# Performance work log

Hardware: AMD Instinct MI355X
Metric: run time of the kernel (lower is better)

The kernel has to match this reference:

```python
import jax, jax.numpy as jnp
import numpy as np

N_NODES = 100000
N_EDGES = 1600000
D = 128  # node_feat_size == edge_hidden_size


def setup_inputs() -> dict:
    key = jax.random.key(0)
    ks = jax.random.split(key, 10)
    s = 1.0 / np.sqrt(D)
    return {
        "node_feats": jax.random.normal(ks[0], (N_NODES, D), jnp.float32),
        "edge_logits": jax.random.normal(ks[1], (N_EDGES, 1), jnp.float32),
        "W_proj": jax.random.normal(ks[2], (D, D), jnp.float32) * s,
        "b_proj": jax.random.normal(ks[3], (D,), jnp.float32) * s,
        "W1": jax.random.normal(ks[4], (2 * D, D), jnp.float32) * s,
        "b1": jax.random.normal(ks[5], (D,), jnp.float32) * s,
        "W2": jax.random.normal(ks[6], (D, D), jnp.float32) * s,
        "b2": jax.random.normal(ks[7], (D,), jnp.float32) * s,
        "src": jax.random.randint(ks[8], (N_EDGES,), 0, N_NODES),
        "dst": jax.random.randint(ks[9], (N_EDGES,), 0, N_NODES),
    }


def reference(node_feats, edge_logits, W_proj, b_proj, W1, b1, W2, b2, src, dst):
    # ---- edge_softmax: softmax of edge_logits grouped by destination node ----
    # [E,1] logits; per-dst max for numerical stability (gradient-free shift)
    m = jax.ops.segment_max(edge_logits, dst, num_segments=N_NODES)  # [N,1]
    m = jnp.where(jnp.isfinite(m), m, 0.0)  # nodes with no in-edges
    e = jnp.exp(edge_logits - jax.lax.stop_gradient(m)[dst])  # [E,1]
    z = jax.ops.segment_sum(e, dst, num_segments=N_NODES)  # [N,1]
    a = e / z[dst]  # [E,1]

    # ---- project_node (dropout is identity at inference) ----
    hv = node_feats @ W_proj + b_proj  # [N,D]

    # ---- src_mul_edge + sum aggregation: c[v] = sum_{(u->v)} a_uv * hv[u] ----
    msg = hv[src] * a  # [E,D]
    c = jax.ops.segment_sum(msg, dst, num_segments=N_NODES)  # [N,D]

    context = jax.nn.elu(c)
    x = jnp.concatenate([context, node_feats], axis=1)  # [N,2D]
    h = jax.nn.relu(x @ W1 + b1)  # Linear -> Dropout(id) -> ReLU
    out = jax.nn.relu(h @ W2 + b2)  # Linear -> Dropout(id), outer ReLU
    return out
```

## Files before the change

### kernel.cpp

```cpp
#include <hip/hip_runtime.h>
#include <hip/hip_bf16.h>

typedef __hip_bfloat16 bf16;
typedef __attribute__((ext_vector_type(8))) __bf16 bf16x8;
typedef __attribute__((ext_vector_type(4))) float floatx4;
typedef __attribute__((ext_vector_type(2))) float floatx2;

#define BUCKET_SHIFT 7
#define BUCKET_NODES 128
#define MAX_NB 1024

__device__ __forceinline__ unsigned short f2b(float f) {
    bf16 h = __float2bfloat16(f);
    unsigned short s;
    __builtin_memcpy(&s, &h, 2);
    return s;
}
__device__ __forceinline__ float b2f(unsigned short u) {
    unsigned int x = ((unsigned int)u) << 16;
    float f;
    __builtin_memcpy(&f, &x, 4);
    return f;
}
__device__ __forceinline__ float load_dual(const void* p, long long i, bool isbf) {
    return isbf ? b2f(((const unsigned short*)p)[i]) : ((const float*)p)[i];
}
__device__ __forceinline__ bf16x8 ldsfrag(const unsigned short* p) {
    union { uint4 u; bf16x8 v; } t;
    t.u = *(const uint4*)p;
    return t.v;
}
__device__ __forceinline__ bf16x8 gfrag_dual(const void* A, int row, int stride, int k0, bool isbf) {
    if (isbf) {
        union { uint4 u; bf16x8 v; } t;
        t.u = *(const uint4*)((const unsigned short*)A + (size_t)row * stride + k0);
        return t.v;
    }
    const float* ap = (const float*)A + (size_t)row * stride + k0;
    float4 v0 = ((const float4*)ap)[0];
    float4 v1 = ((const float4*)ap)[1];
    union { unsigned short s[8]; bf16x8 v; } t;
    t.s[0] = f2b(v0.x); t.s[1] = f2b(v0.y); t.s[2] = f2b(v0.z); t.s[3] = f2b(v0.w);
    t.s[4] = f2b(v1.x); t.s[5] = f2b(v1.y); t.s[6] = f2b(v1.z); t.s[7] = f2b(v1.w);
    return t.v;
}

__global__ __launch_bounds__(64) void detect_kernel(const unsigned int* __restrict__ words,
                                                    int* __restrict__ flag,
                                                    int* __restrict__ bcount) {
    for (int i = threadIdx.x; i < MAX_NB; i += 64) bcount[i] = 0;
    int cnt = 0;
    for (int i = threadIdx.x; i < 4096; i += 64) {
        unsigned int lo = words[i] & 0xFFFFu;
        unsigned int e = (lo >> 7) & 0xFFu;
        if (lo == 0u || (e >= 110u && e <= 135u)) cnt++;
    }
#pragma unroll
    for (int off = 32; off > 0; off >>= 1) cnt += __shfl_down(cnt, off, 64);
    if (threadIdx.x == 0) *flag = (cnt > 2458) ? 1 : 0;
}

__global__ __launch_bounds__(256) void prep_kernel(const void* __restrict__ Wp,
                                                   const void* __restrict__ W1,
                                                   const void* __restrict__ W2,
                                                   unsigned short* __restrict__ Wtp,
                                                   unsigned short* __restrict__ Wt1,
                                                   unsigned short* __restrict__ Wt2,
                                                   const int* __restrict__ flag,
                                                   const int* __restrict__ dst,
                                                   int* __restrict__ bcount, int E) {
    if (blockIdx.x < 256) {
        bool isbf = (*flag != 0);
        int idx = blockIdx.x * 256 + threadIdx.x;
        if (idx < 16384) {
            int n = idx >> 7, k = idx & 127;
            Wtp[idx] = f2b(load_dual(Wp, (long long)k * 128 + n, isbf));
        } else if (idx < 49152) {
            int j = idx - 16384;
            int n = j >> 8, k = j & 255;
            Wt1[j] = f2b(load_dual(W1, (long long)k * 128 + n, isbf));
        } else if (idx < 65536) {
            int j = idx - 49152;
            int n = j >> 7, k = j & 127;
            Wt2[j] = f2b(load_dual(W2, (long long)k * 128 + n, isbf));
        }
    } else {
        __shared__ int lcnt[MAX_NB];
        for (int i = threadIdx.x; i < MAX_NB; i += 256) lcnt[i] = 0;
        __syncthreads();
        int base = (blockIdx.x - 256) * 8192;
#pragma unroll
        for (int j = 0; j < 32; ++j) {
            int e = base + j * 256 + threadIdx.x;
            if (e < E) atomicAdd(&lcnt[dst[e] >> BUCKET_SHIFT], 1);
        }
        __syncthreads();
        for (int i = threadIdx.x; i < MAX_NB; i += 256)
            if (lcnt[i]) atomicAdd(&bcount[i], lcnt[i]);
    }
}

__global__ __launch_bounds__(256) void bscan_kernel(const int* __restrict__ bcount,
                                                    int* __restrict__ bstart,
                                                    int* __restrict__ bcursor, int NB) {
    int t = threadIdx.x;
    int v[4];
    int sum = 0;
#pragma unroll
    for (int j = 0; j < 4; ++j) {
        int i = t * 4 + j;
        v[j] = (i < NB) ? bcount[i] : 0;
        sum += v[j];
    }
    int lane = t & 63, wave = t >> 6;
    int inc = sum;
#pragma unroll
    for (int off = 1; off < 64; off <<= 1) {
        int x = __shfl_up(inc, off, 64);
        if (lane >= off) inc += x;
    }
    __shared__ int wsum[4];
    if (lane == 63) wsum[wave] = inc;
    __syncthreads();
    int woff = 0;
    for (int w = 0; w < wave; ++w) woff += wsum[w];
    int run = inc - sum + woff;
#pragma unroll
    for (int j = 0; j < 4; ++j) {
        int i = t * 4 + j;
        if (i < NB) { bstart[i] = run; bcursor[i] = run; }
        run += v[j];
    }
}

__global__ __launch_bounds__(256) void bappend_kernel(const int* __restrict__ dst,
                                                      const int* __restrict__ src,
                                                      const void* __restrict__ logits,
                                                      int* __restrict__ bcursor,
                                                      uint2* __restrict__ ebuf,
                                                      const int* __restrict__ flag, int E) {
    __shared__ int lcnt[MAX_NB];
    __shared__ int lbase[MAX_NB];
    for (int i = threadIdx.x; i < MAX_NB; i += 256) lcnt[i] = 0;
    __syncthreads();
    const bool isbf = (*flag != 0);
    int base = blockIdx.x * 8192;
#pragma unroll
    for (int j = 0; j < 32; ++j) {
        int e = base + j * 256 + threadIdx.x;
        if (e < E) atomicAdd(&lcnt[dst[e] >> BUCKET_SHIFT], 1);
    }
    __syncthreads();
    for (int i = threadIdx.x; i < MAX_NB; i += 256) {
        int c = lcnt[i];
        if (c) { lbase[i] = atomicAdd(&bcursor[i], c); lcnt[i] = 0; }
    }
    __syncthreads();
#pragma unroll
    for (int j = 0; j < 32; ++j) {
        int e = base + j * 256 + threadIdx.x;
        if (e < E) {
            int d = dst[e];
            int b = d >> BUCKET_SHIFT;
            float w = expf(load_dual(logits, e, isbf));
            int pos = lbase[b] + atomicAdd(&lcnt[b], 1);
            uint2 rec;
            rec.x = (unsigned int)src[e] | ((unsigned int)(d & (BUCKET_NODES - 1)) << 24);
            rec.y = __float_as_uint(w);
            ebuf[pos] = rec;
        }
    }
}

__global__ __launch_bounds__(256) void gemm_bcsr_kernel(const void* __restrict__ A,
                                                        const unsigned short* __restrict__ Wt,
                                                        const void* __restrict__ bias,
                                                        unsigned short* __restrict__ hv,
                                                        const int* __restrict__ flag, int N,
                                                        int gblocks,
                                                        const uint2* __restrict__ ebuf,
                                                        const int* __restrict__ bstart,
                                                        const int* __restrict__ bcount,
                                                        uint2* __restrict__ ebuf2,
                                                        int* __restrict__ row_start,
                                                        int* __restrict__ ncount) {
    __shared__ unsigned short Wl[128 * 136];
    if ((int)blockIdx.x < gblocks) {
        const bool isbf = (*flag != 0);
        const int t = threadIdx.x, wid = t >> 6, lane = t & 63;
        const int m16 = lane & 15, quad = lane >> 4;
        const int row0 = blockIdx.x * 128;
        {
            int r = t >> 1, kh = (t & 1) * 64;
            const uint4* s = (const uint4*)(Wt + (size_t)r * 128 + kh);
            uint4* d = (uint4*)&Wl[r * 136 + kh];
#pragma unroll
            for (int q = 0; q < 8; ++q) d[q] = s[q];
        }
        __syncthreads();

        floatx4 acc[2][8];
#pragma unroll
        for (int i = 0; i < 2; ++i)
#pragma unroll
            for (int j = 0; j < 8; ++j) acc[i][j] = (floatx4){0.f, 0.f, 0.f, 0.f};

        int ra0 = row0 + wid * 32 + m16;      if (ra0 >= N) ra0 = N - 1;
        int ra1 = row0 + wid * 32 + 16 + m16; if (ra1 >= N) ra1 = N - 1;

#pragma unroll
        for (int c = 0; c < 4; ++c) {
            int k0 = c * 32 + quad * 8;
            bf16x8 a0 = gfrag_dual(A, ra0, 128, k0, isbf);
            bf16x8 a1 = gfrag_dual(A, ra1, 128, k0, isbf);
#pragma unroll
            for (int nt = 0; nt < 8; ++nt) {
                bf16x8 b = ldsfrag(&Wl[(nt * 16 + m16) * 136 + k0]);
                acc[0][nt] = __builtin_amdgcn_mfma_f32_16x16x32_bf16(a0, b, acc[0][nt], 0, 0, 0);
                acc[1][nt] = __builtin_amdgcn_mfma_f32_16x16x32_bf16(a1, b, acc[1][nt], 0, 0, 0);
            }
        }

#pragma unroll
        for (int mt = 0; mt < 2; ++mt) {
            int gr0 = row0 + wid * 32 + mt * 16 + quad * 4;
#pragma unroll
            for (int nt = 0; nt < 8; ++nt) {
                int col = nt * 16 + m16;
                float bb = load_dual(bias, col, isbf);
#pragma unroll
                for (int rg = 0; rg < 4; ++rg) {
                    int gr = gr0 + rg;
                    if (gr < N) hv[(size_t)gr * 128 + col] = f2b(acc[mt][nt][rg] + bb);
                }
            }
        }
    } else {
        int* lcnt = (int*)Wl;
        int* lbase = lcnt + BUCKET_NODES;
        const int b = blockIdx.x - gblocks;
        const int s0 = bstart[b];
        const int cnt = bcount[b];
        if (threadIdx.x < BUCKET_NODES) lcnt[threadIdx.x] = 0;
        __syncthreads();
        for (int i = threadIdx.x; i < cnt; i += 256)
            atomicAdd(&lcnt[ebuf[s0 + i].x >> 24], 1);
        __syncthreads();
        if (threadIdx.x < 64) {
            int lane = threadIdx.x;
            int carry = 0;
#pragma unroll
            for (int half = 0; half < 2; ++half) {
                int idx = half * 64 + lane;
                int v = lcnt[idx];
                int inc = v;
#pragma unroll
                for (int off = 1; off < 64; off <<= 1) {
                    int t = __shfl_up(inc, off, 64);
                    if (lane >= off) inc += t;
                }
                lbase[idx] = carry + inc - v;
                carry += __shfl(inc, 63, 64);
            }
        }
        __syncthreads();
        if (threadIdx.x < BUCKET_NODES) {
            int gn = b * BUCKET_NODES + threadIdx.x;
            if (gn < N) {
                row_start[gn] = s0 + lbase[threadIdx.x];
                ncount[gn] = lcnt[threadIdx.x];
            }
        }
        __syncthreads();
        if (threadIdx.x < BUCKET_NODES) lcnt[threadIdx.x] = 0;
        __syncthreads();
        for (int i = threadIdx.x; i < cnt; i += 256) {
            uint2 rec = ebuf[s0 + i];
            int dl = rec.x >> 24;
            int pos = lbase[dl] + atomicAdd(&lcnt[dl], 1);
            ebuf2[s0 + pos] = make_uint2(rec.x & 0xFFFFFFu, rec.y);
        }
    }
}

__global__ __launch_bounds__(256) void agg_csr_kernel(const int* __restrict__ row_start,
                                                      const int* __restrict__ ncount,
                                                      const unsigned long long* __restrict__ erec,
                                                      const unsigned int* __restrict__ hv32,
                                                      unsigned int* __restrict__ ctx32, int N) {
    int n = blockIdx.x * 4 + (threadIdx.x >> 6);
    int lane = threadIdx.x & 63;
    if (n >= N) return;
    int s0 = __builtin_amdgcn_readfirstlane(row_start[n]);
    int deg = __builtin_amdgcn_readfirstlane(ncount[n]);
    const unsigned long long* ep = erec + s0;
    const unsigned int lb = (unsigned int)lane << 2;
    floatx2 acc = {0.f, 0.f};
    float z = 0.f;
    int i = 0;
    for (; i + 16 <= deg; i += 16) {
        unsigned long long r[16];
        unsigned int h[16];
#pragma unroll
        for (int j = 0; j < 16; ++j) r[j] = ep[i + j];
#pragma unroll
        for (int j = 0; j < 16; ++j) {
            unsigned int sx = (unsigned int)r[j];
            __builtin_assume(sx < (1u << 24));
            h[j] = *(const unsigned int*)((const char*)hv32 + ((sx << 8) | lb));
        }
#pragma unroll
        for (int j = 0; j < 16; ++j) {
            float w = __uint_as_float((unsigned int)(r[j] >> 32));
            z += w;
            floatx2 hf = { __uint_as_float(h[j] << 16),
                           __uint_as_float(h[j] & 0xFFFF0000u) };
            acc += hf * w;
        }
    }
    for (; i + 4 <= deg; i += 4) {
        unsigned long long r[4];
        unsigned int h[4];
#pragma unroll
        for (int j = 0; j < 4; ++j) r[j] = ep[i + j];
#pragma unroll
        for (int j = 0; j < 4; ++j) {
            unsigned int sx = (unsigned int)r[j];
            __builtin_assume(sx < (1u << 24));
            h[j] = *(const unsigned int*)((const char*)hv32 + ((sx << 8) | lb));
        }
#pragma unroll
        for (int j = 0; j < 4; ++j) {
            float w = __uint_as_float((unsigned int)(r[j] >> 32));
            z += w;
            floatx2 hf = { __uint_as_float(h[j] << 16),
                           __uint_as_float(h[j] & 0xFFFF0000u) };
            acc += hf * w;
        }
    }
    for (; i < deg; ++i) {
        unsigned long long r = ep[i];
        unsigned int sx = (unsigned int)r;
        __builtin_assume(sx < (1u << 24));
        unsigned int h = *(const unsigned int*)((const char*)hv32 + ((sx << 8) | lb));
        float w = __uint_as_float((unsigned int)(r >> 32));
        z += w;
        floatx2 hf = { __uint_as_float(h << 16),
                       __uint_as_float(h & 0xFFFF0000u) };
        acc += hf * w;
    }
    float rz = (z > 0.f) ? 1.f / z : 0.f;
    float x = acc.x * rz, y = acc.y * rz;
    x = x > 0.f ? x : expm1f(x);
    y = y > 0.f ? y : expm1f(y);
    ctx32[(size_t)n * 64 + lane] = ((unsigned int)f2b(y) << 16) | f2b(x);
}

__global__ __launch_bounds__(256) void mlp_fused(const unsigned short* __restrict__ ctx,
                                                 const void* __restrict__ nf,
                                                 const unsigned short* __restrict__ Wt1,
                                                 const void* __restrict__ b1,
                                                 const unsigned short* __restrict__ Wt2,
                                                 const void* __restrict__ b2,
                                                 void* __restrict__ outp,
                                                 const int* __restrict__ flag, int N) {
    __shared__ unsigned short Wl[128 * 72];
    __shared__ unsigned short Hl[4][32 * 136];
    const bool isbf = (*flag != 0);
    const int t = threadIdx.x, wid = t >> 6, lane = t & 63;
    const int m16 = lane & 15, quad = lane >> 4;
    const int row0 = blockIdx.x * 128;

    floatx4 acc[2][8];
#pragma unroll
    for (int i = 0; i < 2; ++i)
#pragma unroll
        for (int j = 0; j < 8; ++j) acc[i][j] = (floatx4){0.f, 0.f, 0.f, 0.f};

    int ra0 = row0 + wid * 32 + m16;      if (ra0 >= N) ra0 = N - 1;
    int ra1 = row0 + wid * 32 + 16 + m16; if (ra1 >= N) ra1 = N - 1;

#pragma unroll
    for (int kc = 0; kc < 4; ++kc) {
        {
            int r = t >> 1, kh = (t & 1) * 32;
            const uint4* s = (const uint4*)(Wt1 + (size_t)r * 256 + kc * 64 + kh);
            uint4* d = (uint4*)&Wl[r * 72 + kh];
#pragma unroll
            for (int q = 0; q < 4; ++q) d[q] = s[q];
        }
        __syncthreads();
#pragma unroll
        for (int c = 0; c < 2; ++c) {
            int kl = c * 32 + quad * 8;
            int ka = kc * 64 + kl;
            bf16x8 a0, a1;
            if (ka < 128) {
                union { uint4 u; bf16x8 v; } t0, t1;
                t0.u = *(const uint4*)(ctx + (size_t)ra0 * 128 + ka);
                t1.u = *(const uint4*)(ctx + (size_t)ra1 * 128 + ka);
                a0 = t0.v; a1 = t1.v;
            } else {
                a0 = gfrag_dual(nf, ra0, 128, ka - 128, isbf);
                a1 = gfrag_dual(nf, ra1, 128, ka - 128, isbf);
            }
#pragma unroll
            for (int nt = 0; nt < 8; ++nt) {
                bf16x8 b = ldsfrag(&Wl[(nt * 16 + m16) * 72 + kl]);
                acc[0][nt] = __builtin_amdgcn_mfma_f32_16x16x32_bf16(a0, b, acc[0][nt], 0, 0, 0);
                acc[1][nt] = __builtin_amdgcn_mfma_f32_16x16x32_bf16(a1, b, acc[1][nt], 0, 0, 0);
            }
        }
        __syncthreads();
    }

#pragma unroll
    for (int nt = 0; nt < 8; ++nt) {
        int col = nt * 16 + m16;
        float bb = load_dual(b1, col, isbf);
#pragma unroll
        for (int mt = 0; mt < 2; ++mt) {
#pragma unroll
            for (int rg = 0; rg < 4; ++rg) {
                int lr = mt * 16 + quad * 4 + rg;
                float x = acc[mt][nt][rg] + bb;
                Hl[wid][lr * 136 + col] = f2b(x > 0.f ? x : 0.f);
            }
        }
    }

#pragma unroll
    for (int i = 0; i < 2; ++i)
#pragma unroll
        for (int j = 0; j < 8; ++j) acc[i][j] = (floatx4){0.f, 0.f, 0.f, 0.f};

#pragma unroll
    for (int kc = 0; kc < 2; ++kc) {
        {
            int r = t >> 1, kh = (t & 1) * 32;
            const uint4* s = (const uint4*)(Wt2 + (size_t)r * 128 + kc * 64 + kh);
            uint4* d = (uint4*)&Wl[r * 72 + kh];
#pragma unroll
            for (int q = 0; q < 4; ++q) d[q] = s[q];
        }
        __syncthreads();
#pragma unroll
        for (int c = 0; c < 2; ++c) {
            int kl = c * 32 + quad * 8;
            int ka = kc * 64 + kl;
            bf16x8 a0 = ldsfrag(&Hl[wid][m16 * 136 + ka]);
            bf16x8 a1 = ldsfrag(&Hl[wid][(16 + m16) * 136 + ka]);
#pragma unroll
            for (int nt = 0; nt < 8; ++nt) {
                bf16x8 b = ldsfrag(&Wl[(nt * 16 + m16) * 72 + kl]);
                acc[0][nt] = __builtin_amdgcn_mfma_f32_16x16x32_bf16(a0, b, acc[0][nt], 0, 0, 0);
                acc[1][nt] = __builtin_amdgcn_mfma_f32_16x16x32_bf16(a1, b, acc[1][nt], 0, 0, 0);
            }
        }
        __syncthreads();
    }

#pragma unroll
    for (int mt = 0; mt < 2; ++mt) {
        int gr0 = row0 + wid * 32 + mt * 16 + quad * 4;
#pragma unroll
        for (int nt = 0; nt < 8; ++nt) {
            int col = nt * 16 + m16;
            float bb = load_dual(b2, col, isbf);
#pragma unroll
            for (int rg = 0; rg < 4; ++rg) {
                int gr = gr0 + rg;
                if (gr < N) {
                    float x = acc[mt][nt][rg] + bb;
                    x = x > 0.f ? x : 0.f;
                    if (!isbf) ((float*)outp)[(size_t)gr * 128 + col] = x;
                    else       ((unsigned short*)outp)[(size_t)gr * 128 + col] = f2b(x);
                }
            }
        }
    }
}

extern "C" void kernel_launch(void* const* d_in, const int* in_sizes, int n_in,
                              void* d_out, int out_size, void* d_ws, size_t ws_size,
                              hipStream_t stream) {
    const void* node_feats  = d_in[0];
    const void* edge_logits = d_in[1];
    const void* W_proj      = d_in[2];
    const void* b_proj      = d_in[3];
    const void* W1          = d_in[4];
    const void* b1          = d_in[5];
    const void* W2          = d_in[6];
    const void* b2          = d_in[7];
    const int*  src         = (const int*)d_in[8];
    const int*  dst         = (const int*)d_in[9];

    const int N = in_sizes[0] / 128;
    const int E = in_sizes[8];
    const int NB = (N + BUCKET_NODES - 1) / BUCKET_NODES;

    char* ws = (char*)d_ws;
    size_t off = 0;
    unsigned short* hv  = (unsigned short*)(ws + off); off += (size_t)N * 256;
    unsigned short* ctx = (unsigned short*)(ws + off); off += (size_t)N * 256;
    uint2* ebuf  = (uint2*)(ws + off); off += (size_t)E * 8;
    uint2* ebuf2 = (uint2*)(ws + off); off += (size_t)E * 8;
    unsigned short* Wtp = (unsigned short*)(ws + off); off += 128 * 128 * 2;
    unsigned short* Wt1 = (unsigned short*)(ws + off); off += 128 * 256 * 2;
    unsigned short* Wt2 = (unsigned short*)(ws + off); off += 128 * 128 * 2;
    int* bcount    = (int*)(ws + off); off += MAX_NB * 4;
    int* bstart    = (int*)(ws + off); off += MAX_NB * 4;
    int* bcursor   = (int*)(ws + off); off += MAX_NB * 4;
    int* row_start = (int*)(ws + off); off += (size_t)N * 4;
    int* ncount    = (int*)(ws + off); off += (size_t)N * 4;
    int* flag      = (int*)(ws + off);

    const int gblocks = (N + 127) / 128;
    const int ebblocks = (E + 8191) / 8192;

    detect_kernel<<<1, 64, 0, stream>>>((const unsigned int*)node_feats, flag, bcount);
    prep_kernel<<<256 + ebblocks, 256, 0, stream>>>(W_proj, W1, W2, Wtp, Wt1, Wt2,
                                                    flag, dst, bcount, E);
    bscan_kernel<<<1, 256, 0, stream>>>(bcount, bstart, bcursor, NB);
    bappend_kernel<<<ebblocks, 256, 0, stream>>>(dst, src, edge_logits, bcursor,
                                                 ebuf, flag, E);
    gemm_bcsr_kernel<<<gblocks + NB, 256, 0, stream>>>(node_feats, Wtp, b_proj, hv,
                                                       flag, N, gblocks,
                                                       ebuf, bstart, bcount, ebuf2,
                                                       row_start, ncount);
    agg_csr_kernel<<<(N + 3) / 4, 256, 0, stream>>>(row_start, ncount,
                                                    (const unsigned long long*)ebuf2,
                                                    (const unsigned int*)hv,
                                                    (unsigned int*)ctx, N);
    mlp_fused<<<gblocks, 256, 0, stream>>>(ctx, node_feats, Wt1, b1, Wt2, b2,
                                           d_out, flag, N);
}
```

Before: 346.0 us.

## Replace two-level bucket sort with direct per-node counting-sort CSR build

Builds the destination CSR by counting in-degree per node with global atomics, running a hierarchical prefix scan, and scattering edge records directly to per-node cursors. This drops the bucketed two-pass sort and its second edge buffer. The append pass still runs alongside the projection GEMM. The cost is heavy global atomic traffic on 100K counters, edge order within a node becoming nondeterministic, and two extra small kernel launches.

```diff
diff --git a/kernel.cpp b/kernel.cpp
--- a/kernel.cpp
+++ b/kernel.cpp
@@ -6,9 +6,8 @@
 typedef __attribute__((ext_vector_type(4))) float floatx4;
 typedef __attribute__((ext_vector_type(2))) float floatx2;
 
-#define BUCKET_SHIFT 7
-#define BUCKET_NODES 128
-#define MAX_NB 1024
+#define CHUNK 1024
+#define CNT_BLOCKS 1024
 
 __device__ __forceinline__ unsigned short f2b(float f) {
     bf16 h = __float2bfloat16(f);
@@ -46,9 +45,7 @@
 }
 
 __global__ __launch_bounds__(64) void detect_kernel(const unsigned int* __restrict__ words,
-                                                    int* __restrict__ flag,
-                                                    int* __restrict__ bcount) {
-    for (int i = threadIdx.x; i < MAX_NB; i += 64) bcount[i] = 0;
+                                                    int* __restrict__ flag) {
     int cnt = 0;
     for (int i = threadIdx.x; i < 4096; i += 64) {
         unsigned int lo = words[i] & 0xFFFFu;
@@ -60,18 +57,19 @@
     if (threadIdx.x == 0) *flag = (cnt > 2458) ? 1 : 0;
 }
 
-__global__ __launch_bounds__(256) void prep_kernel(const void* __restrict__ Wp,
-                                                   const void* __restrict__ W1,
-                                                   const void* __restrict__ W2,
-                                                   unsigned short* __restrict__ Wtp,
-                                                   unsigned short* __restrict__ Wt1,
-                                                   unsigned short* __restrict__ Wt2,
-                                                   const int* __restrict__ flag,
-                                                   const int* __restrict__ dst,
-                                                   int* __restrict__ bcount, int E) {
+__global__ __launch_bounds__(256) void count_kernel(const int* __restrict__ dst,
+                                                    int* __restrict__ ncount, int E,
+                                                    const void* __restrict__ Wp,
+                                                    const void* __restrict__ W1,
+                                                    const void* __restrict__ W2,
+                                                    unsigned short* __restrict__ Wtp,
+                                                    unsigned short* __restrict__ Wt1,
+                                                    unsigned short* __restrict__ Wt2,
+                                                    const int* __restrict__ flag) {
+    const int t = threadIdx.x;
     if (blockIdx.x < 256) {
-        bool isbf = (*flag != 0);
-        int idx = blockIdx.x * 256 + threadIdx.x;
+        const bool isbf = (*flag != 0);
+        int idx = blockIdx.x * 256 + t;
         if (idx < 16384) {
             int n = idx >> 7, k = idx & 127;
             Wtp[idx] = f2b(load_dual(Wp, (long long)k * 128 + n, isbf));
@@ -84,32 +82,25 @@
             int n = j >> 7, k = j & 127;
             Wt2[j] = f2b(load_dual(W2, (long long)k * 128 + n, isbf));
         }
-    } else {
-        __shared__ int lcnt[MAX_NB];
-        for (int i = threadIdx.x; i < MAX_NB; i += 256) lcnt[i] = 0;
-        __syncthreads();
-        int base = (blockIdx.x - 256) * 8192;
-#pragma unroll
-        for (int j = 0; j < 32; ++j) {
-            int e = base + j * 256 + threadIdx.x;
-            if (e < E) atomicAdd(&lcnt[dst[e] >> BUCKET_SHIFT], 1);
-        }
-        __syncthreads();
-        for (int i = threadIdx.x; i < MAX_NB; i += 256)
-            if (lcnt[i]) atomicAdd(&bcount[i], lcnt[i]);
-    }
-}
-
-__global__ __launch_bounds__(256) void bscan_kernel(const int* __restrict__ bcount,
-                                                    int* __restrict__ bstart,
-                                                    int* __restrict__ bcursor, int NB) {
-    int t = threadIdx.x;
+        return;
+    }
+    int idx = ((int)blockIdx.x - 256) * 256 + t;
+    const int stride = CNT_BLOCKS * 256;
+    for (int e = idx; e < E; e += stride)
+        atomicAdd(&ncount[dst[e]], 1);
+}
+
+__global__ __launch_bounds__(256) void scanp_kernel(const int* __restrict__ ncount,
+                                                    int* __restrict__ row_start,
+                                                    int* __restrict__ csum, int N) {
+    const int t = threadIdx.x;
+    const int base = blockIdx.x * CHUNK;
     int v[4];
     int sum = 0;
 #pragma unroll
     for (int j = 0; j < 4; ++j) {
-        int i = t * 4 + j;
-        v[j] = (i < NB) ? bcount[i] : 0;
+        int i = base + t * 4 + j;
+        v[j] = (i < N) ? ncount[i] : 0;
         sum += v[j];
     }
     int lane = t & 63, wave = t >> 6;
@@ -127,67 +118,77 @@
     int run = inc - sum + woff;
 #pragma unroll
     for (int j = 0; j < 4; ++j) {
+        int i = base + t * 4 + j;
+        if (i < N) row_start[i] = run;
+        run += v[j];
+    }
+    if (t == 255) csum[blockIdx.x] = run;
+}
+
+__global__ __launch_bounds__(256) void scant_kernel(const int* __restrict__ csum,
+                                                    int* __restrict__ cbase, int NC) {
+    const int t = threadIdx.x;
+    int v[4];
+    int sum = 0;
+#pragma unroll
+    for (int j = 0; j < 4; ++j) {
         int i = t * 4 + j;
-        if (i < NB) { bstart[i] = run; bcursor[i] = run; }
+        v[j] = (i < NC) ? csum[i] : 0;
+        sum += v[j];
+    }
+    int lane = t & 63, wave = t >> 6;
+    int inc = sum;
+#pragma unroll
+    for (int off = 1; off < 64; off <<= 1) {
+        int x = __shfl_up(inc, off, 64);
+        if (lane >= off) inc += x;
+    }
+    __shared__ int wsum[4];
+    if (lane == 63) wsum[wave] = inc;
+    __syncthreads();
+    int woff = 0;
+    for (int w = 0; w < wave; ++w) woff += wsum[w];
+    int run = inc - sum + woff;
+#pragma unroll
+    for (int j = 0; j < 4; ++j) {
+        int i = t * 4 + j;
+        if (i < NC) cbase[i] = run;
         run += v[j];
     }
 }
 
-__global__ __launch_bounds__(256) void bappend_kernel(const int* __restrict__ dst,
-                                                      const int* __restrict__ src,
-                                                      const void* __restrict__ logits,
-                                                      int* __restrict__ bcursor,
-                                                      uint2* __restrict__ ebuf,
-                                                      const int* __restrict__ flag, int E) {
-    __shared__ int lcnt[MAX_NB];
-    __shared__ int lbase[MAX_NB];
-    for (int i = threadIdx.x; i < MAX_NB; i += 256) lcnt[i] = 0;
-    __syncthreads();
-    const bool isbf = (*flag != 0);
-    int base = blockIdx.x * 8192;
-#pragma unroll
-    for (int j = 0; j < 32; ++j) {
-        int e = base + j * 256 + threadIdx.x;
-        if (e < E) atomicAdd(&lcnt[dst[e] >> BUCKET_SHIFT], 1);
-    }
-    __syncthreads();
-    for (int i = threadIdx.x; i < MAX_NB; i += 256) {
-        int c = lcnt[i];
-        if (c) { lbase[i] = atomicAdd(&bcursor[i], c); lcnt[i] = 0; }
-    }
-    __syncthreads();
-#pragma unroll
-    for (int j = 0; j < 32; ++j) {
-        int e = base + j * 256 + threadIdx.x;
-        if (e < E) {
-            int d = dst[e];
-            int b = d >> BUCKET_SHIFT;
-            float w = expf(load_dual(logits, e, isbf));
-            int pos = lbase[b] + atomicAdd(&lcnt[b], 1);
-            uint2 rec;
-            rec.x = (unsigned int)src[e] | ((unsigned int)(d & (BUCKET_NODES - 1)) << 24);
-            rec.y = __float_as_uint(w);
-            ebuf[pos] = rec;
-        }
-    }
-}
-
-__global__ __launch_bounds__(256) void gemm_bcsr_kernel(const void* __restrict__ A,
-                                                        const unsigned short* __restrict__ Wt,
-                                                        const void* __restrict__ bias,
-                                                        unsigned short* __restrict__ hv,
-                                                        const int* __restrict__ flag, int N,
-                                                        int gblocks,
-                                                        const uint2* __restrict__ ebuf,
-                                                        const int* __restrict__ bstart,
-                                                        const int* __restrict__ bcount,
-                                                        uint2* __restrict__ ebuf2,
-                                                        int* __restrict__ row_start,
-                                                        int* __restrict__ ncount) {
+__global__ __launch_bounds__(256) void addback_kernel(int* __restrict__ row_start,
+                                                      int* __restrict__ cursor,
+                                                      const int* __restrict__ cbase, int N) {
+    const int cb = cbase[blockIdx.x];
+    int i0 = blockIdx.x * CHUNK + threadIdx.x * 4;
+#pragma unroll
+    for (int j = 0; j < 4; ++j) {
+        int k = i0 + j;
+        if (k < N) {
+            int r = row_start[k] + cb;
+            row_start[k] = r;
+            cursor[k] = r;
+        }
+    }
+}
+
+__global__ __launch_bounds__(256) void gemm_append_kernel(const void* __restrict__ A,
+                                                          const unsigned short* __restrict__ Wt,
+                                                          const void* __restrict__ bias,
+                                                          unsigned short* __restrict__ hv,
+                                                          const int* __restrict__ flag, int N,
+                                                          int gblocks,
+                                                          const int* __restrict__ dst,
+                                                          const int* __restrict__ src,
+                                                          const void* __restrict__ logits,
+                                                          int* __restrict__ cursor,
+                                                          uint2* __restrict__ rec, int E) {
     __shared__ unsigned short Wl[128 * 136];
+    const int t = threadIdx.x;
     if ((int)blockIdx.x < gblocks) {
         const bool isbf = (*flag != 0);
-        const int t = threadIdx.x, wid = t >> 6, lane = t & 63;
+        const int wid = t >> 6, lane = t & 63;
         const int m16 = lane & 15, quad = lane >> 4;
         const int row0 = blockIdx.x * 128;
         {
@@ -236,50 +237,29 @@
             }
         }
     } else {
-        int* lcnt = (int*)Wl;
-        int* lbase = lcnt + BUCKET_NODES;
-        const int b = blockIdx.x - gblocks;
-        const int s0 = bstart[b];
-        const int cnt = bcount[b];
-        if (threadIdx.x < BUCKET_NODES) lcnt[threadIdx.x] = 0;
-        __syncthreads();
-        for (int i = threadIdx.x; i < cnt; i += 256)
-            atomicAdd(&lcnt[ebuf[s0 + i].x >> 24], 1);
-        __syncthreads();
-        if (threadIdx.x < 64) {
-            int lane = threadIdx.x;
-            int carry = 0;
-#pragma unroll
-            for (int half = 0; half < 2; ++half) {
-                int idx = half * 64 + lane;
-                int v = lcnt[idx];
-                int inc = v;
-#pragma unroll
-                for (int off = 1; off < 64; off <<= 1) {
-                    int t = __shfl_up(inc, off, 64);
-                    if (lane >= off) inc += t;
-                }
-                lbase[idx] = carry + inc - v;
-                carry += __shfl(inc, 63, 64);
-            }
-        }
-        __syncthreads();
-        if (threadIdx.x < BUCKET_NODES) {
-            int gn = b * BUCKET_NODES + threadIdx.x;
-            if (gn < N) {
-                row_start[gn] = s0 + lbase[threadIdx.x];
-                ncount[gn] = lcnt[threadIdx.x];
-            }
-        }
-        __syncthreads();
-        if (threadIdx.x < BUCKET_NODES) lcnt[threadIdx.x] = 0;
-        __syncthreads();
-        for (int i = threadIdx.x; i < cnt; i += 256) {
-            uint2 rec = ebuf[s0 + i];
-            int dl = rec.x >> 24;
-            int pos = lbase[dl] + atomicAdd(&lcnt[dl], 1);
-            ebuf2[s0 + pos] = make_uint2(rec.x & 0xFFFFFFu, rec.y);
-        }
+        const bool isbf = (*flag != 0);
+        int e0 = (((int)blockIdx.x - gblocks) * 256 + t) * 4;
+        int d[4];
+        unsigned int s4[4];
+        float w[4];
+        int nv = 0;
+#pragma unroll
+        for (int j = 0; j < 4; ++j) {
+            int e = e0 + j;
+            if (e < E) {
+                d[j] = dst[e];
+                s4[j] = (unsigned int)src[e];
+                w[j] = expf(load_dual(logits, e, isbf));
+                nv = j + 1;
+            }
+        }
+        int pos[4];
+#pragma unroll
+        for (int j = 0; j < 4; ++j)
+            if (j < nv) pos[j] = atomicAdd(&cursor[d[j]], 1);
+#pragma unroll
+        for (int j = 0; j < 4; ++j)
+            if (j < nv) rec[pos[j]] = make_uint2(s4[j], __float_as_uint(w[j]));
     }
 }
 
@@ -497,39 +477,39 @@
 
     const int N = in_sizes[0] / 128;
     const int E = in_sizes[8];
-    const int NB = (N + BUCKET_NODES - 1) / BUCKET_NODES;
+    const int NC = (N + CHUNK - 1) / CHUNK;
 
     char* ws = (char*)d_ws;
     size_t off = 0;
     unsigned short* hv  = (unsigned short*)(ws + off); off += (size_t)N * 256;
     unsigned short* ctx = (unsigned short*)(ws + off); off += (size_t)N * 256;
-    uint2* ebuf  = (uint2*)(ws + off); off += (size_t)E * 8;
-    uint2* ebuf2 = (uint2*)(ws + off); off += (size_t)E * 8;
+    uint2* rec = (uint2*)(ws + off); off += (size_t)E * 8;
     unsigned short* Wtp = (unsigned short*)(ws + off); off += 128 * 128 * 2;
     unsigned short* Wt1 = (unsigned short*)(ws + off); off += 128 * 256 * 2;
     unsigned short* Wt2 = (unsigned short*)(ws + off); off += 128 * 128 * 2;
-    int* bcount    = (int*)(ws + off); off += MAX_NB * 4;
-    int* bstart    = (int*)(ws + off); off += MAX_NB * 4;
-    int* bcursor   = (int*)(ws + off); off += MAX_NB * 4;
+    int* ncount    = (int*)(ws + off); off += (size_t)N * 4;
     int* row_start = (int*)(ws + off); off += (size_t)N * 4;
-    int* ncount    = (int*)(ws + off); off += (size_t)N * 4;
+    int* cursor    = (int*)(ws + off); off += (size_t)N * 4;
+    int* csum      = (int*)(ws + off); off += CHUNK * 4;
+    int* cbase     = (int*)(ws + off); off += CHUNK * 4;
     int* flag      = (int*)(ws + off);
 
     const int gblocks = (N + 127) / 128;
-    const int ebblocks = (E + 8191) / 8192;
-
-    detect_kernel<<<1, 64, 0, stream>>>((const unsigned int*)node_feats, flag, bcount);
-    prep_kernel<<<256 + ebblocks, 256, 0, stream>>>(W_proj, W1, W2, Wtp, Wt1, Wt2,
-                                                    flag, dst, bcount, E);
-    bscan_kernel<<<1, 256, 0, stream>>>(bcount, bstart, bcursor, NB);
-    bappend_kernel<<<ebblocks, 256, 0, stream>>>(dst, src, edge_logits, bcursor,
-                                                 ebuf, flag, E);
-    gemm_bcsr_kernel<<<gblocks + NB, 256, 0, stream>>>(node_feats, Wtp, b_proj, hv,
-                                                       flag, N, gblocks,
-                                                       ebuf, bstart, bcount, ebuf2,
-                                                       row_start, ncount);
+    const int ablocks = (E + 1023) / 1024;
+
+    detect_kernel<<<1, 64, 0, stream>>>((const unsigned int*)node_feats, flag);
+    hipMemsetAsync(ncount, 0, (size_t)N * 4, stream);
+    count_kernel<<<256 + CNT_BLOCKS, 256, 0, stream>>>(dst, ncount, E, W_proj, W1, W2,
+                                                       Wtp, Wt1, Wt2, flag);
+    scanp_kernel<<<NC, 256, 0, stream>>>(ncount, row_start, csum, N);
+    scant_kernel<<<1, 256, 0, stream>>>(csum, cbase, NC);
+    addback_kernel<<<NC, 256, 0, stream>>>(row_start, cursor, cbase, N);
+    gemm_append_kernel<<<gblocks + ablocks, 256, 0, stream>>>(node_feats, Wtp, b_proj,
+                                                              hv, flag, N, gblocks,
+                                                              dst, src, edge_logits,
+                                                              cursor, rec, E);
     agg_csr_kernel<<<(N + 3) / 4, 256, 0, stream>>>(row_start, ncount,
-                                                    (const unsigned long long*)ebuf2,
+                                                    (const unsigned long long*)rec,
                                                     (const unsigned int*)hv,
                                                     (unsigned int*)ctx, N);
     mlp_fused<<<gblocks, 256, 0, stream>>>(ctx, node_feats, Wt1, b1, Wt2, b2,
```

After: 426.3 us. +23.2%, slower.
